# Optimization experiments

Measured on AMD Instinct MI355X. Metric: run time of the kernel, lower is better.

## Reference

```python
import jax, jax.numpy as jnp
import numpy as np

B, J, O = 32, 20, 20
D, H, F, L = 256, 8, 1024, 6
S = J * O
DH = D // H
NL = L + 1  # 6 encoder blocks + final block stacked together


def setup_inputs() -> dict:
    ks = jax.random.split(jax.random.key(0), 16)
    s = 0.02
    am = jax.random.randint(ks[4], (B, J), 0, 2) == 1
    am = am.at[:, 0].set(False)  # at least one unmasked job per row (avoid all -inf softmax)
    return {
        "operations": jax.random.normal(ks[0], (B, J, O, 2), jnp.float32),
        "job_ops_mask": jax.random.normal(ks[1], (B, J, O, O), jnp.float32),
        "ops_machines_mask": jax.random.normal(ks[2], (B, S, S), jnp.float32),
        "jobs_next_op_idx": jax.random.randint(ks[3], (B, J, 1), 0, O),
        "action_mask": am,
        "qkv_w": jax.random.normal(ks[5], (NL, 3 * D, D), jnp.float32) * s,
        "qkv_b": jnp.zeros((NL, 3 * D), jnp.float32),
        "out_w": jax.random.normal(ks[6], (NL, D, D), jnp.float32) * s,
        "out_b": jnp.zeros((NL, D), jnp.float32),
        "ln1_g": jnp.ones((NL, D), jnp.float32),
        "ln1_b": jnp.zeros((NL, D), jnp.float32),
        "ln2_g": jnp.ones((NL, D), jnp.float32),
        "ln2_b": jnp.zeros((NL, D), jnp.float32),
        "ff1_w": jax.random.normal(ks[7], (NL, F, D), jnp.float32) * s,
        "ff1_b": jnp.zeros((NL, F), jnp.float32),
        "ff2_w": jax.random.normal(ks[8], (NL, D, F), jnp.float32) * s,
        "ff2_b": jnp.zeros((NL, D), jnp.float32),
        "op_emb_w": jax.random.normal(ks[9], (D, 2), jnp.float32) * s,
        "op_emb_b": jnp.zeros((D,), jnp.float32),
        "pol_w": jax.random.normal(ks[10], (1, D), jnp.float32) * s,
        "pol_b": jnp.zeros((1,), jnp.float32),
    }


def _ln(x, g, b):
    m = x.mean(-1, keepdims=True)
    v = ((x - m) ** 2).mean(-1, keepdims=True)
    return (x - m) * jax.lax.rsqrt(v + 1e-5) * g + b


def _mha(x, mask, qw, qb, ow, ob):
    N, Sq, _ = x.shape
    qkv = x @ qw.T + qb
    q, k, v = jnp.split(qkv, 3, axis=-1)
    q = q.reshape(N, Sq, H, DH).transpose(0, 2, 1, 3)
    k = k.reshape(N, Sq, H, DH).transpose(0, 2, 1, 3)
    v = v.reshape(N, Sq, H, DH).transpose(0, 2, 1, 3)
    sc = jnp.einsum("nhqd,nhkd->nhqk", q, k) / jnp.sqrt(jnp.float32(DH))
    sc = sc + mask  # additive float attn mask, broadcast over heads where needed
    a = jax.nn.softmax(sc, axis=-1)
    o = jnp.einsum("nhqk,nhkd->nhqd", a, v).transpose(0, 2, 1, 3).reshape(N, Sq, D)
    return o @ ow.T + ob


def _forward(operations, job_ops_mask, ops_machines_mask, jobs_next_op_idx, action_mask,
             qkv_w, qkv_b, out_w, out_b, ln1_g, ln1_b, ln2_g, ln2_b,
             ff1_w, ff1_b, ff2_w, ff2_b, op_emb_w, op_emb_b, pol_w, pol_b):
    def block(x, mask, i):  # pre-norm TransformerEncoderLayer, gelu, dropout=0
        h = _ln(x, ln1_g[i], ln1_b[i])
        x = x + _mha(h, mask, qkv_w[i], qkv_b[i], out_w[i], out_b[i])
        h = _ln(x, ln2_g[i], ln2_b[i])
        ff = jax.nn.gelu(h @ ff1_w[i].T + ff1_b[i], approximate=False) @ ff2_w[i].T + ff2_b[i]
        return x + ff

    # sinusoidal positional encoding over the operation index
    pos = jnp.arange(O, dtype=jnp.float32)[:, None]
    div = jnp.exp(jnp.arange(0, D, 2, dtype=jnp.float32) * (-np.log(10000.0) / D))
    pe = jnp.stack([jnp.sin(pos * div), jnp.cos(pos * div)], axis=-1).reshape(O, D)
    x = operations @ op_emb_w.T + op_emb_b + pe[None, None]  # (B,J,O,D)

    # ALiBi slopes: 1/x^(i+1), x = 256^(1/H)
    base = (2.0 ** 8) ** (1.0 / H)
    slope = (1.0 / base ** jnp.arange(1, H + 1, dtype=jnp.float32))[None, :, None, None]
    job_mask = job_ops_mask.reshape(B * J, 1, O, O) * slope  # (B*J, H, O, O)
    mach_mask = ops_machines_mask[:, None, :, :]  # (B, 1, S, S), identical across heads

    for i in range(L):
        if i % 2 == 0:  # per-job attention over operations
            x = block(x.reshape(B * J, O, D), job_mask, i).reshape(B, J, O, D)
        else:  # per-machine attention over all operations
            x = block(x.reshape(B, S, D), mach_mask, i).reshape(B, J, O, D)

    idx = jnp.broadcast_to(jobs_next_op_idx[:, :, :, None], (B, J, 1, D))
    nxt = jnp.take_along_axis(x, idx, axis=2)[:, :, 0, :]  # (B, J, D)
    kp = jnp.where(action_mask, -jnp.inf, 0.0)[:, None, None, :]  # key padding mask
    nxt = block(nxt, kp, L)
    logits = (nxt @ pol_w.T + pol_b)[:, :, 0]
    return jnp.where(action_mask, -jnp.inf, logits)


def reference(operations, job_ops_mask, ops_machines_mask, jobs_next_op_idx, action_mask,
              qkv_w, qkv_b, out_w, out_b, ln1_g, ln1_b, ln2_g, ln2_b,
              ff1_w, ff1_b, ff2_w, ff2_b, op_emb_w, op_emb_b, pol_w, pol_b):
    return _forward(operations, job_ops_mask, ops_machines_mask, jobs_next_op_idx, action_mask,
                    qkv_w, qkv_b, out_w, out_b, ln1_g, ln1_b, ln2_g, ln2_b,
                    ff1_w, ff1_b, ff2_w, ff2_b, op_emb_w, op_emb_b, pol_w, pol_b)
```

## Files before the change

### kernel.cpp

```cpp
#include <hip/hip_runtime.h>
#include <math.h>

#define B_  32
#define J_  20
#define O_  20
#define S_  400
#define D_  256
#define H_  8
#define F_  1024
#define L_  6
#define T_  12800
#define T2_ 640

#define NEG_BIG (-1e30f)

typedef __attribute__((ext_vector_type(8))) short short8;
typedef __attribute__((ext_vector_type(4))) float f32x4;

__device__ __forceinline__ short f2b(float f) {
  union { float f; unsigned u; } c; c.f = f;
  unsigned r = (c.u + 0x7FFFu + ((c.u >> 16) & 1u)) >> 16;
  return (short)r;
}
__device__ __forceinline__ float b2f(short s) {
  union { unsigned u; float f; } c;
  c.u = ((unsigned)(unsigned short)s) << 16;
  return c.f;
}
__device__ __forceinline__ unsigned addpk(unsigned a, unsigned b) {
  union { unsigned u; float f; } x, y;
  x.u = a << 16;        y.u = b << 16;        float lo = x.f + y.f;
  x.u = a & 0xffff0000u; y.u = b & 0xffff0000u; float hi = x.f + y.f;
  return (unsigned)(unsigned short)f2b(lo) | ((unsigned)(unsigned short)f2b(hi) << 16);
}
__device__ __forceinline__ void async_copy16(const short* g, short* l) {
  __builtin_amdgcn_global_load_lds(
      (const __attribute__((address_space(1))) void*)g,
      (__attribute__((address_space(3))) void*)l, 16, 0, 0);
}

__global__ __launch_bounds__(256) void k_f2b4(
    const float* __restrict__ s0, short* __restrict__ d0,
    const float* __restrict__ s1, short* __restrict__ d1,
    const float* __restrict__ s2, short* __restrict__ d2,
    const float* __restrict__ s3, short* __restrict__ d3,
    const float* __restrict__ s4, short* __restrict__ d4)
{
  int bid = blockIdx.x;
  const float* src; short* dst; int base;
  if (bid < 672)        { src = s0; dst = d0; base = bid; }
  else if (bid < 896)   { src = s1; dst = d1; base = bid - 672; }
  else if (bid < 1792)  { src = s2; dst = d2; base = bid - 896; }
  else if (bid < 2688)  { src = s3; dst = d3; base = bid - 1792; }
  else                  { src = s4; dst = d4; base = bid - 2688; }
  int i = (base * 256 + threadIdx.x) * 8;
  float4 a = *(const float4*)(src + i);
  float4 b = *(const float4*)(src + i + 4);
  short8 o;
  o[0] = f2b(a.x); o[1] = f2b(a.y); o[2] = f2b(a.z); o[3] = f2b(a.w);
  o[4] = f2b(b.x); o[5] = f2b(b.y); o[6] = f2b(b.z); o[7] = f2b(b.w);
  *(short8*)(dst + i) = o;
}

__global__ __launch_bounds__(640) void k_maskconv(
    const void* __restrict__ am_raw, int* __restrict__ am_out)
{
  __shared__ int isInt32;
  const int tid = threadIdx.x;
  if (tid == 0) isInt32 = 1;
  __syncthreads();
  if (tid < 160) {
    int v = ((const int*)am_raw)[tid];
    if (v != 0 && v != 1) atomicAnd(&isInt32, 0);
  }
  __syncthreads();
  if (tid < 640) {
    int v;
    if (isInt32) v = ((const int*)am_raw)[tid] != 0;
    else         v = ((const unsigned char*)am_raw)[tid] != 0;
    am_out[tid] = v;
  }
}

__global__ __launch_bounds__(256) void k_embed(
    const float* __restrict__ ops, const float* __restrict__ ew,
    const float* __restrict__ eb, short* __restrict__ x)
{
  int idx = blockIdx.x * 256 + threadIdx.x;
  int d = idx & 255;
  int t = idx >> 8;
  int o = t % O_;
  float a0 = ops[(size_t)t * 2 + 0], a1 = ops[(size_t)t * 2 + 1];
  int k = d >> 1;
  float div = expf((float)(2 * k) * -0.03597789207803197f);
  float ang = (float)o * div;
  float pe = (d & 1) ? cosf(ang) : sinf(ang);
  x[idx] = f2b(a0 * ew[d * 2 + 0] + a1 * ew[d * 2 + 1] + eb[d] + pe);
}

__global__ __launch_bounds__(256) void k_ln(
    const short* __restrict__ x, const float* __restrict__ g, const float* __restrict__ b,
    short* __restrict__ out, int nTok)
{
  int gid = blockIdx.x * 256 + threadIdx.x;
  int tok = gid >> 6, lane = threadIdx.x & 63;
  if (tok >= nTok) return;
  int2 pk = ((const int2*)(x + (size_t)tok * 256))[lane];
  union { unsigned u; float f; } c;
  float vx, vy, vz, vw;
  c.u = (unsigned)pk.x << 16;        vx = c.f;
  c.u = (unsigned)pk.x & 0xffff0000u; vy = c.f;
  c.u = (unsigned)pk.y << 16;        vz = c.f;
  c.u = (unsigned)pk.y & 0xffff0000u; vw = c.f;
  float s = vx + vy + vz + vw;
  #pragma unroll
  for (int off = 32; off > 0; off >>= 1) s += __shfl_down(s, off);
  float mean = __shfl(s, 0) * (1.f / 256.f);
  float dx = vx - mean, dy = vy - mean, dz = vz - mean, dw = vw - mean;
  float q = dx * dx + dy * dy + dz * dz + dw * dw;
  #pragma unroll
  for (int off = 32; off > 0; off >>= 1) q += __shfl_down(q, off);
  float var = __shfl(q, 0) * (1.f / 256.f);
  float inv = 1.f / sqrtf(var + 1e-5f);
  float4 gv = ((const float4*)g)[lane];
  float4 bv = ((const float4*)b)[lane];
  float ox = dx * inv * gv.x + bv.x;
  float oy = dy * inv * gv.y + bv.y;
  float oz = dz * inv * gv.z + bv.z;
  float ow = dw * inv * gv.w + bv.w;
  int2 po;
  po.x = (int)(unsigned short)f2b(ox) | ((int)(unsigned short)f2b(oy) << 16);
  po.y = (int)(unsigned short)f2b(oz) | ((int)(unsigned short)f2b(ow) << 16);
  ((int2*)(out + (size_t)tok * 256))[lane] = po;
}

__global__ __launch_bounds__(256) void k_gemm_bf16(
    const short* __restrict__ A, const short* __restrict__ W,
    const float* __restrict__ bias, const short* __restrict__ R,
    short* __restrict__ C, int M, int N, int K, int act)
{
  __shared__ short LDS_[17408];
  short* Asf = LDS_;
  short* Bsf = LDS_ + 8192;
  short* Csf = LDS_;
  const int tid  = threadIdx.x;
  const int lane = tid & 63;
  const int wv   = tid >> 6;
  const int lm   = lane & 15;
  const int quad = lane >> 4;
  const int wm   = (wv >> 1) * 64;
  const int wn   = (wv & 1) * 64;
  const int n0 = blockIdx.x * 128;
  const int m0 = blockIdx.y * 128;

  f32x4 acc[4][4] = {};

  for (int k0 = 0; k0 < K; k0 += 64) {
    __syncthreads();
    #pragma unroll
    for (int i = 0; i < 4; ++i) {
      const int c    = tid + 256 * i;
      const int row  = c >> 3;
      const int kc8  = ((c & 7) ^ (row & 7)) * 8;
      async_copy16(A + (size_t)(m0 + row) * K + k0 + kc8, &Asf[c * 8]);
      async_copy16(W + (size_t)(n0 + row) * K + k0 + kc8, &Bsf[c * 8]);
    }
    __syncthreads();
    #pragma unroll
    for (int kh = 0; kh < 2; ++kh) {
      short8 af[4], bf[4];
      #pragma unroll
      for (int i = 0; i < 4; ++i) {
        const int row  = wm + i * 16 + lm;
        const int slot = (kh * 4 + quad) ^ (lm & 7);
        af[i] = *(short8*)&Asf[(row * 8 + slot) * 8];
      }
      #pragma unroll
      for (int j = 0; j < 4; ++j) {
        const int row  = wn + j * 16 + lm;
        const int slot = (kh * 4 + quad) ^ (lm & 7);
        bf[j] = *(short8*)&Bsf[(row * 8 + slot) * 8];
      }
      #pragma unroll
      for (int i = 0; i < 4; ++i)
        #pragma unroll
        for (int j = 0; j < 4; ++j)
          acc[i][j] = __builtin_amdgcn_mfma_f32_16x16x32_bf16(af[i], bf[j], acc[i][j], 0, 0, 0);
    }
  }

  __syncthreads();
  #pragma unroll
  for (int j = 0; j < 4; ++j) {
    const int ccol = wn + j * 16 + lm;
    const float bv = bias[n0 + ccol];
    #pragma unroll
    for (int i = 0; i < 4; ++i) {
      #pragma unroll
      for (int r = 0; r < 4; ++r) {
        const int row = wm + i * 16 + quad * 4 + r;
        float vvv = acc[i][j][r] + bv;
        if (act) vvv = vvv / (1.f + __expf(-1.702f * vvv));
        Csf[row * 136 + ccol] = f2b(vvv);
      }
    }
  }
  __syncthreads();
  {
    const int srow = tid >> 1, sh = (tid & 1) * 64;
    const size_t gbase = (size_t)(m0 + srow) * N + n0 + sh;
    const short* ls = &Csf[srow * 136 + sh];
    #pragma unroll
    for (int u = 0; u < 8; ++u) {
      uint4 v = *(const uint4*)(ls + u * 8);
      if (R) {
        uint4 rv = *(const uint4*)(R + gbase + u * 8);
        v.x = addpk(v.x, rv.x); v.y = addpk(v.y, rv.y);
        v.z = addpk(v.z, rv.z); v.w = addpk(v.w, rv.w);
      }
      *(uint4*)(C + gbase + u * 8) = v;
    }
  }
}

__global__ __launch_bounds__(256) void k_gemm_ln(
    const short* __restrict__ A, const short* __restrict__ W,
    const float* __restrict__ bias, const short* __restrict__ R,
    short* __restrict__ X, short* __restrict__ Hout,
    const float* __restrict__ g, const float* __restrict__ bb_,
    int M, int K)
{
  __shared__ short LDS_[4096 + 16896];
  short* Asf = LDS_;
  short* Bsf = LDS_ + 4096;
  short* Csf = LDS_ + 4096;
  const int tid  = threadIdx.x;
  const int lane = tid & 63;
  const int wv   = tid >> 6;
  const int lm   = lane & 15;
  const int quad = lane >> 4;
  const int wn   = wv * 64;
  const int m0   = blockIdx.x * 64;

  f32x4 acc[4][4] = {};

  for (int k0 = 0; k0 < K; k0 += 64) {
    __syncthreads();
    #pragma unroll
    for (int i = 0; i < 2; ++i) {
      const int c   = tid + 256 * i;
      const int row = c >> 3;
      const int kc8 = ((c & 7) ^ (row & 7)) * 8;
      async_copy16(A + (size_t)(m0 + row) * K + k0 + kc8, &Asf[c * 8]);
    }
    #pragma unroll
    for (int i = 0; i < 8; ++i) {
      const int c   = tid + 256 * i;
      const int row = c >> 3;
      const int kc8 = ((c & 7) ^ (row & 7)) * 8;
      async_copy16(W + (size_t)row * K + k0 + kc8, &Bsf[c * 8]);
    }
    __syncthreads();
    #pragma unroll
    for (int kh = 0; kh < 2; ++kh) {
      short8 af[4], bf[4];
      #pragma unroll
      for (int i = 0; i < 4; ++i) {
        const int row  = i * 16 + lm;
        const int slot = (kh * 4 + quad) ^ (lm & 7);
        af[i] = *(short8*)&Asf[(row * 8 + slot) * 8];
      }
      #pragma unroll
      for (int j = 0; j < 4; ++j) {
        const int row  = wn + j * 16 + lm;
        const int slot = (kh * 4 + quad) ^ (lm & 7);
        bf[j] = *(short8*)&Bsf[(row * 8 + slot) * 8];
      }
      #pragma unroll
      for (int i = 0; i < 4; ++i)
        #pragma unroll
        for (int j = 0; j < 4; ++j)
          acc[i][j] = __builtin_amdgcn_mfma_f32_16x16x32_bf16(af[i], bf[j], acc[i][j], 0, 0, 0);
    }
  }

  __syncthreads();
  #pragma unroll
  for (int j = 0; j < 4; ++j) {
    const int ccol = wn + j * 16 + lm;
    const float bv = bias[ccol];
    #pragma unroll
    for (int i = 0; i < 4; ++i) {
      #pragma unroll
      for (int r = 0; r < 4; ++r) {
        const int row = i * 16 + quad * 4 + r;
        Csf[row * 264 + ccol] = f2b(acc[i][j][r] + bv);
      }
    }
  }
  __syncthreads();

  {
    const int row = tid >> 2, cb = (tid & 3) * 64;
    const size_t gbase = (size_t)(m0 + row) * 256 + cb;
    const short* ls = &Csf[row * 264 + cb];
    uint4 xv[8];
    float s1 = 0.f, s2 = 0.f;
    #pragma unroll
    for (int u = 0; u < 8; ++u) {
      uint4 v = *(const uint4*)(ls + u * 8);
      uint4 rv = *(const uint4*)(R + gbase + u * 8);
      v.x = addpk(v.x, rv.x); v.y = addpk(v.y, rv.y);
      v.z = addpk(v.z, rv.z); v.w = addpk(v.w, rv.w);
      xv[u] = v;
      *(uint4*)(X + gbase + u * 8) = v;
      #pragma unroll
      for (int w2 = 0; w2 < 4; ++w2) {
        unsigned pv = (&v.x)[w2];
        union { unsigned u; float f; } c1, c2;
        c1.u = pv << 16; c2.u = pv & 0xffff0000u;
        s1 += c1.f + c2.f;
        s2 += c1.f * c1.f + c2.f * c2.f;
      }
    }
    s1 += __shfl_xor(s1, 1); s2 += __shfl_xor(s2, 1);
    s1 += __shfl_xor(s1, 2); s2 += __shfl_xor(s2, 2);
    const float mean = s1 * (1.f / 256.f);
    const float var  = s2 * (1.f / 256.f) - mean * mean;
    const float inv  = 1.f / sqrtf(var + 1e-5f);
    #pragma unroll
    for (int u = 0; u < 8; ++u) {
      float4 g0 = *(const float4*)(g + cb + u * 8);
      float4 g1 = *(const float4*)(g + cb + u * 8 + 4);
      float4 b0 = *(const float4*)(bb_ + cb + u * 8);
      float4 b1 = *(const float4*)(bb_ + cb + u * 8 + 4);
      auto lnpk = [&](unsigned pv, float ga, float gb2, float ba, float bb2) -> unsigned {
        union { unsigned u; float f; } c1, c2;
        c1.u = pv << 16; c2.u = pv & 0xffff0000u;
        float lo = (c1.f - mean) * inv * ga + ba;
        float hi = (c2.f - mean) * inv * gb2 + bb2;
        return (unsigned)(unsigned short)f2b(lo) | ((unsigned)(unsigned short)f2b(hi) << 16);
      };
      uint4 hv;
      hv.x = lnpk(xv[u].x, g0.x, g0.y, b0.x, b0.y);
      hv.y = lnpk(xv[u].y, g0.z, g0.w, b0.z, b0.w);
      hv.z = lnpk(xv[u].z, g1.x, g1.y, b1.x, b1.y);
      hv.w = lnpk(xv[u].w, g1.z, g1.w, b1.z, b1.w);
      *(uint4*)(Hout + gbase + u * 8) = hv;
    }
  }
}

#define QSTR 776
#define PSTR20 40
__global__ __launch_bounds__(512) void k_attn20_mfma(
    const short* __restrict__ qkv, short* __restrict__ att,
    const float* __restrict__ jmask, const int* __restrict__ amask, int mode)
{
  __shared__ short QK[32 * QSTR];
  __shared__ short Ps[8][32 * PSTR20];
  const int seq  = blockIdx.x;
  const int tid  = threadIdx.x;
  const int wv   = tid >> 6;
  const int lane = tid & 63;
  const int l15  = lane & 15;
  const int quad = lane >> 4;
  const float scale = 0.1767766952966369f;

  for (int e = tid; e < 3072; e += 512) {
    int row = e / 96, c8 = (e % 96) * 8;
    uint4 v = {0u, 0u, 0u, 0u};
    if (row < 20) v = *(const uint4*)(qkv + ((size_t)seq * 20 + row) * 768 + c8);
    *(uint4*)&QK[row * QSTR + c8] = v;
  }
  __syncthreads();

  const short8 aq0 = *(short8*)&QK[(0  + l15) * QSTR + wv * 32 + quad * 8];
  const short8 aq1 = *(short8*)&QK[(16 + l15) * QSTR + wv * 32 + quad * 8];
  const short8 bk0 = *(short8*)&QK[(0  + l15) * QSTR + 256 + wv * 32 + quad * 8];
  const short8 bk1 = *(short8*)&QK[(16 + l15) * QSTR + 256 + wv * 32 + quad * 8];
  f32x4 z4 = {0.f, 0.f, 0.f, 0.f};
  f32x4 s00 = __builtin_amdgcn_mfma_f32_16x16x32_bf16(aq0, bk0, z4, 0, 0, 0);
  f32x4 s01 = __builtin_amdgcn_mfma_f32_16x16x32_bf16(aq0, bk1, z4, 0, 0, 0);
  f32x4 s10 = __builtin_amdgcn_mfma_f32_16x16x32_bf16(aq1, bk0, z4, 0, 0, 0);
  f32x4 s11 = __builtin_amdgcn_mfma_f32_16x16x32_bf16(aq1, bk1, z4, 0, 0, 0);

  const float slope = exp2f(-(float)(wv + 1));
  short* psw = &Ps[wv][0];
  float l0[4] = {0.f, 0.f, 0.f, 0.f};
  float l1[4] = {0.f, 0.f, 0.f, 0.f};

  #pragma unroll
  for (int kt = 0; kt < 2; ++kt) {
    const int k  = kt * 16 + l15;
    const int kc = (k < 20) ? k : 19;
    float madd1 = 0.f;
    if (mode == 1) madd1 = amask[seq * 20 + kc] ? NEG_BIG : 0.f;
    #pragma unroll
    for (int qt = 0; qt < 2; ++qt) {
      f32x4 s = (kt == 0) ? (qt == 0 ? s00 : s10) : (qt == 0 ? s01 : s11);
      #pragma unroll
      for (int r = 0; r < 4; ++r) {
        const int q  = qt * 16 + quad * 4 + r;
        const int qc = (q < 20) ? q : 19;
        float sv = s[r] * scale;
        if (mode == 0) sv += jmask[(size_t)seq * 400 + qc * 20 + kc] * slope;
        else           sv += madd1;
        float p = (k < 20) ? __expf(fminf(sv, 40.f)) : 0.f;
        if (qt == 0) l0[r] += p; else l1[r] += p;
        psw[q * PSTR20 + k] = f2b(p);
      }
    }
  }
  #pragma unroll
  for (int r = 0; r < 4; ++r) {
    float t0 = l0[r];
    t0 += __shfl_xor(t0, 1); t0 += __shfl_xor(t0, 2);
    t0 += __shfl_xor(t0, 4); t0 += __shfl_xor(t0, 8);
    l0[r] = 1.f / t0;
    float t1 = l1[r];
    t1 += __shfl_xor(t1, 1); t1 += __shfl_xor(t1, 2);
    t1 += __shfl_xor(t1, 4); t1 += __shfl_xor(t1, 8);
    l1[r] = 1.f / t1;
  }

  const short8 pf0 = *(short8*)&psw[(0  + l15) * PSTR20 + quad * 8];
  const short8 pf1 = *(short8*)&psw[(16 + l15) * PSTR20 + quad * 8];
  #pragma unroll
  for (int dt = 0; dt < 2; ++dt) {
    const int d = wv * 32 + dt * 16 + l15;
    short8 vf;
    #pragma unroll
    for (int j = 0; j < 8; ++j)
      vf[j] = QK[(quad * 8 + j) * QSTR + 512 + d];
    f32x4 o0 = __builtin_amdgcn_mfma_f32_16x16x32_bf16(pf0, vf, z4, 0, 0, 0);
    f32x4 o1 = __builtin_amdgcn_mfma_f32_16x16x32_bf16(pf1, vf, z4, 0, 0, 0);
    #pragma unroll
    for (int r = 0; r < 4; ++r) {
      const int q = quad * 4 + r;
      att[((size_t)seq * 20 + q) * 256 + d] = f2b(o0[r] * l0[r]);
    }
    if (quad == 0) {
      #pragma unroll
      for (int r = 0; r < 4; ++r) {
        const int q = 16 + r;
        att[((size_t)seq * 20 + q) * 256 + d] = f2b(o1[r] * l1[r]);
      }
    }
  }
}

#define VTS 416
__global__ __launch_bounds__(256) void k_vtrans(
    const short* __restrict__ qkv, short* __restrict__ vt)
{
  __shared__ short T[64][73];
  const int bid = blockIdx.x;
  const int b  = bid / 28, rem = bid % 28;
  const int kt = rem / 4, dt = rem % 4;
  const int k0 = kt * 64, d0 = dt * 64;
  const int tid = threadIdx.x;
  #pragma unroll
  for (int i = 0; i < 2; ++i) {
    const int c = tid + 256 * i;
    const int row = c >> 3, cc = (c & 7) * 8;
    const int tok = k0 + row;
    uint4 v = {0u, 0u, 0u, 0u};
    if (tok < 400)
      v = *(const uint4*)(qkv + ((size_t)(b * 400 + tok)) * 768 + 512 + d0 + cc);
    *(uint4*)&T[row][cc] = v;
  }
  __syncthreads();
  #pragma unroll
  for (int i = 0; i < 2; ++i) {
    const int c = tid + 256 * i;
    const int dl = c >> 3, kk = (c & 7) * 8;
    if (k0 + kk < VTS) {
      short8 o;
      #pragma unroll
      for (int j = 0; j < 8; ++j) o[j] = T[kk + j][dl];
      *(short8*)(vt + ((size_t)(b * 256 + d0 + dl)) * VTS + k0 + kk) = o;
    }
  }
}

#define PSTRW 40
#define MSTR 424
__global__ __launch_bounds__(512) void k_attn400_mfma(
    const short* __restrict__ qkv, const short* __restrict__ vt,
    short* __restrict__ att, const short* __restrict__ mbf)
{
  __shared__ short Pl[8][16 * PSTRW];
  __shared__ short Ml[16 * MSTR];

  const int id   = blockIdx.x;
  const int b    = (id >> 3) / 25 * 8 + (id & 7);
  const int qt   = (id >> 3) % 25;
  const int tid  = threadIdx.x;
  const int wv   = tid >> 6;
  const int lane = tid & 63;
  const int l15  = lane & 15;
  const int quad = lane >> 4;
  const int q0   = qt * 16;
  const float scale = 0.1767766952966369f;

  for (int e = tid; e < 16 * 52; e += 512) {
    const int row = e / 52, cc = e % 52;
    uint4 v = {0u, 0u, 0u, 0u};
    if (cc < 50)
      v = *(const uint4*)(mbf + ((size_t)(b * 400 + q0 + row)) * 400 + cc * 8);
    *(uint4*)&Ml[row * MSTR + cc * 8] = v;
  }

  short* Pw = &Pl[wv][0];
  const short* qbase = qkv + (size_t)b * 400 * 768;
  const short* vtb   = vt + ((size_t)b * 256 + wv * 32) * VTS;

  const short8 af = *(const short8*)(qbase + (size_t)(q0 + l15) * 768 + wv * 32 + quad * 8);

  f32x4 accO[2] = {};
  float lsum = 0.f;

  short8 kf0, kf1, nvf0, nvf1;
  auto prefK = [&](int k0) {
    kf0 = *(const short8*)(qbase + (size_t)(k0 + l15) * 768 + 256 + wv * 32 + quad * 8);
    int kr = k0 + 16 + l15; if (kr > 399) kr = 399;
    kf1 = *(const short8*)(qbase + (size_t)kr * 768 + 256 + wv * 32 + quad * 8);
  };
  auto prefV = [&](int k0) {
    nvf0 = *(const short8*)(vtb + (size_t)(0  + l15) * VTS + k0 + quad * 8);
    nvf1 = *(const short8*)(vtb + (size_t)(16 + l15) * VTS + k0 + quad * 8);
  };
  prefK(0);
  prefV(0);

  __syncthreads();

  const short* mrow = &Ml[l15 * MSTR];

  for (int k0 = 0; k0 < 416; k0 += 32) {
    const short8 ck0 = kf0, ck1 = kf1;
    const short8 cv0 = nvf0, cv1 = nvf1;

    f32x4 z4 = {0.f, 0.f, 0.f, 0.f};
    f32x4 s0 = __builtin_amdgcn_mfma_f32_16x16x32_bf16(ck0, af, z4, 0, 0, 0);
    f32x4 s1 = __builtin_amdgcn_mfma_f32_16x16x32_bf16(ck1, af, z4, 0, 0, 0);

    if (k0 + 32 < 416) { prefK(k0 + 32); prefV(k0 + 32); }

    uint2 ma = *(const uint2*)(mrow + k0 + quad * 4);
    uint2 mb = *(const uint2*)(mrow + k0 + 16 + quad * 4);
    float mAv[4], mBv[4];
    {
      union { unsigned u; float f; } c;
      c.u = ma.x << 16;         mAv[0] = c.f;
      c.u = ma.x & 0xffff0000u; mAv[1] = c.f;
      c.u = ma.y << 16;         mAv[2] = c.f;
      c.u = ma.y & 0xffff0000u; mAv[3] = c.f;
      c.u = mb.x << 16;         mBv[0] = c.f;
      c.u = mb.x & 0xffff0000u; mBv[1] = c.f;
      c.u = mb.y << 16;         mBv[2] = c.f;
      c.u = mb.y & 0xffff0000u; mBv[3] = c.f;
    }

    float p0[4], p1[4];
    #pragma unroll
    for (int r = 0; r < 4; ++r) {
      const int kB = k0 + 16 + quad * 4 + r;
      float svA = s0[r] * scale + mAv[r];
      float svB = (kB < 400) ? (s1[r] * scale + mBv[r]) : NEG_BIG;
      p0[r] = __expf(fminf(svA, 40.f));
      p1[r] = __expf(fminf(svB, 40.f));
      lsum += p0[r] + p1[r];
    }

    unsigned pk00, pk01, pk10, pk11;
    asm("v_cvt_pk_bf16_f32 %0, %1, %2" : "=v"(pk00) : "v"(p0[0]), "v"(p0[1]));
    asm("v_cvt_pk_bf16_f32 %0, %1, %2" : "=v"(pk01) : "v"(p0[2]), "v"(p0[3]));
    asm("v_cvt_pk_bf16_f32 %0, %1, %2" : "=v"(pk10) : "v"(p1[0]), "v"(p1[1]));
    asm("v_cvt_pk_bf16_f32 %0, %1, %2" : "=v"(pk11) : "v"(p1[2]), "v"(p1[3]));
    uint2 w0; w0.x = pk00; w0.y = pk01;
    uint2 w1; w1.x = pk10; w1.y = pk11;
    *(uint2*)&Pw[l15 * PSTRW + quad * 4]      = w0;
    *(uint2*)&Pw[l15 * PSTRW + 16 + quad * 4] = w1;
    const short8 pf = *(short8*)&Pw[l15 * PSTRW + quad * 8];

    accO[0] = __builtin_amdgcn_mfma_f32_16x16x32_bf16(cv0, pf, accO[0], 0, 0, 0);
    accO[1] = __builtin_amdgcn_mfma_f32_16x16x32_bf16(cv1, pf, accO[1], 0, 0, 0);
  }

  lsum += __shfl_xor(lsum, 16);
  lsum += __shfl_xor(lsum, 32);
  const float inv = 1.f / lsum;

  #pragma unroll
  for (int c = 0; c < 2; ++c) {
    float a0 = accO[c][0] * inv, a1 = accO[c][1] * inv;
    float a2 = accO[c][2] * inv, a3 = accO[c][3] * inv;
    unsigned o01, o23;
    asm("v_cvt_pk_bf16_f32 %0, %1, %2" : "=v"(o01) : "v"(a0), "v"(a1));
    asm("v_cvt_pk_bf16_f32 %0, %1, %2" : "=v"(o23) : "v"(a2), "v"(a3));
    uint2 ov; ov.x = o01; ov.y = o23;
    *(uint2*)&att[((size_t)b * 400 + q0 + l15) * 256 + wv * 32 + c * 16 + quad * 4] = ov;
  }
}

__global__ __launch_bounds__(256) void k_gather2(
    const short* __restrict__ x, const short* __restrict__ h,
    const int* __restrict__ idx, short* __restrict__ x2, short* __restrict__ h2)
{
  int t = blockIdx.x * 256 + threadIdx.x;
  if (t >= 640 * 16) return;
  int bj = t >> 4, c = t & 15;
  int o = idx[bj];
  size_t src = ((size_t)bj * 20 + o) * 256;
  ((uint4*)(x2 + (size_t)bj * 256))[c] = ((const uint4*)(x + src))[c];
  ((uint4*)(h2 + (size_t)bj * 256))[c] = ((const uint4*)(h + src))[c];
}

__global__ __launch_bounds__(256) void k_logits(
    const short* __restrict__ x2, const float* __restrict__ pw, const float* __restrict__ pb,
    const int* __restrict__ am, float* __restrict__ out)
{
  int gid = blockIdx.x * 256 + threadIdx.x;
  int row = gid >> 6, lane = threadIdx.x & 63;
  int2 pk = ((const int2*)(x2 + (size_t)row * 256))[lane];
  union { unsigned u; float f; } c;
  float vx, vy, vz, vw;
  c.u = (unsigned)pk.x << 16;         vx = c.f;
  c.u = (unsigned)pk.x & 0xffff0000u; vy = c.f;
  c.u = (unsigned)pk.y << 16;         vz = c.f;
  c.u = (unsigned)pk.y & 0xffff0000u; vw = c.f;
  float4 w = ((const float4*)pw)[lane];
  float s = vx * w.x + vy * w.y + vz * w.z + vw * w.w;
  #pragma unroll
  for (int off = 32; off > 0; off >>= 1) s += __shfl_down(s, off);
  if (lane == 0) out[row] = am[row] ? NEG_BIG : (s + pb[0]);
}

extern "C" void kernel_launch(void* const* d_in, const int* in_sizes, int n_in,
                              void* d_out, int out_size, void* d_ws, size_t ws_size,
                              hipStream_t stream)
{
  (void)in_sizes; (void)n_in; (void)out_size; (void)ws_size;
  const float* operations        = (const float*)d_in[0];
  const float* job_ops_mask      = (const float*)d_in[1];
  const float* ops_machines_mask = (const float*)d_in[2];
  const int*   jobs_next_op_idx  = (const int*)d_in[3];
  const void*  action_mask_raw   = (const void*)d_in[4];
  const float* qkv_w = (const float*)d_in[5];
  const float* qkv_b = (const float*)d_in[6];
  const float* out_w = (const float*)d_in[7];
  const float* out_b = (const float*)d_in[8];
  const float* ln1_g = (const float*)d_in[9];
  const float* ln1_b = (const float*)d_in[10];
  const float* ln2_g = (const float*)d_in[11];
  const float* ln2_b = (const float*)d_in[12];
  const float* ff1_w = (const float*)d_in[13];
  const float* ff1_b = (const float*)d_in[14];
  const float* ff2_w = (const float*)d_in[15];
  const float* ff2_b = (const float*)d_in[16];
  const float* op_emb_w = (const float*)d_in[17];
  const float* op_emb_b = (const float*)d_in[18];
  const float* pol_w = (const float*)d_in[19];
  const float* pol_b = (const float*)d_in[20];
  float* out = (float*)d_out;

  short* x    = (short*)d_ws;
  short* x2   = x + (size_t)T_ * D_;
  short* h    = x2 + (size_t)T2_ * D_;
  short* big  = h + (size_t)T_ * D_;
  short* h2   = big + (size_t)T_ * F_;
  short* big2 = h2 + (size_t)T2_ * D_;
  int*   amc  = (int*)(big2 + (size_t)T2_ * F_);
  short* bwq  = (short*)(amc + 640);
  short* bwo  = bwq + (size_t)7 * 768 * 256;
  short* bwf1 = bwo + (size_t)7 * 256 * 256;
  short* bwf2 = bwf1 + (size_t)7 * 1024 * 256;
  short* mbf  = bwf2 + (size_t)7 * 256 * 1024;
  short* vt   = mbf + (size_t)B_ * 400 * 400;

  auto gemm = [&](const short* A, const short* Wb, const float* bias, const short* R,
                  short* C, int M, int N, int K, int act) {
    k_gemm_bf16<<<dim3(N / 128, M / 128), dim3(256), 0, stream>>>(
        A, Wb, bias, R, C, M, N, K, act);
  };
  auto gemm_ln = [&](const short* A, const short* Wb, const float* bias, const short* R,
                     short* X, short* Hout, const float* g, const float* b, int M, int K) {
    k_gemm_ln<<<dim3(M / 64), dim3(256), 0, stream>>>(
        A, Wb, bias, R, X, Hout, g, b, M, K);
  };

  k_f2b4<<<dim3(5188), 256, 0, stream>>>(qkv_w, bwq, out_w, bwo, ff1_w, bwf1,
                                         ff2_w, bwf2, ops_machines_mask, mbf);
  k_maskconv<<<dim3(1), dim3(640), 0, stream>>>(action_mask_raw, amc);
  k_embed<<<dim3(T_ * D_ / 256), dim3(256), 0, stream>>>(operations, op_emb_w, op_emb_b, x);
  k_ln<<<dim3(T_ / 4), 256, 0, stream>>>(x, ln1_g, ln1_b, h, T_);

  for (int i = 0; i < L_; ++i) {
    const short* qw  = bwq  + (size_t)i * 768 * 256;
    const float* qb  = qkv_b + (size_t)i * 768;
    const short* ow  = bwo  + (size_t)i * 256 * 256;
    const float* ob  = out_b + (size_t)i * 256;
    const short* f1w = bwf1 + (size_t)i * 1024 * 256;
    const float* f1b = ff1_b + (size_t)i * 1024;
    const short* f2w = bwf2 + (size_t)i * 256 * 1024;
    const float* f2b_ = ff2_b + (size_t)i * 256;
    gemm(h, qw, qb, nullptr, big, T_, 768, 256, 0);
    if ((i & 1) == 0) {
      k_attn20_mfma<<<dim3(640), 512, 0, stream>>>(big, h, job_ops_mask, nullptr, 0);
    } else {
      k_vtrans<<<dim3(896), 256, 0, stream>>>(big, vt);
      k_attn400_mfma<<<dim3(800), 512, 0, stream>>>(big, vt, h, mbf);
    }
    gemm_ln(h, ow, ob, x, x, h, ln2_g + i * D_, ln2_b + i * D_, T_, 256);
    gemm(h, f1w, f1b, nullptr, big, T_, 1024, 256, 1);
    gemm_ln(big, f2w, f2b_, x, x, h, ln1_g + (i + 1) * D_, ln1_b + (i + 1) * D_, T_, 1024);
  }

  k_gather2<<<dim3(40), 256, 0, stream>>>(x, h, jobs_next_op_idx, x2, h2);

  {
    int i = L_;
    const short* qw  = bwq  + (size_t)i * 768 * 256;
    const float* qb  = qkv_b + (size_t)i * 768;
    const short* ow  = bwo  + (size_t)i * 256 * 256;
    const float* ob  = out_b + (size_t)i * 256;
    const short* f1w = bwf1 + (size_t)i * 1024 * 256;
    const float* f1b = ff1_b + (size_t)i * 1024;
    const short* f2w = bwf2 + (size_t)i * 256 * 1024;
    const float* f2b_ = ff2_b + (size_t)i * 256;
    gemm(h2, qw, qb, nullptr, big2, T2_, 768, 256, 0);
    k_attn20_mfma<<<dim3(32), 512, 0, stream>>>(big2, h2, nullptr, amc, 1);
    gemm_ln(h2, ow, ob, x2, x2, h2, ln2_g + i * D_, ln2_b + i * D_, T2_, 256);
    gemm(h2, f1w, f1b, nullptr, big2, T2_, 1024, 256, 1);
    gemm(big2, f2w, f2b_, x2, x2, T2_, 256, 1024, 0);
  }

  k_logits<<<dim3(160), 256, 0, stream>>>(x2, pol_w, pol_b, amc, out);
}
```

Baseline: 961.0 us.

## Process 32 queries per block in 400-token attention with double-buffered K/V prefetch

The per-machine attention kernel now handles two 16-row query tiles per block. Each loaded K and V fragment is reused for two query tiles, which halves K/V global traffic per query and cuts the grid from 800 to 416 blocks. K/V prefetch becomes two-deep, alternating buffers across a manually unrolled loop. In exchange, each thread holds more registers and there are fewer blocks to fill the GPU. The last tile of 16 padded rows does redundant work, and those rows are clamped on load and masked on store.

After: 931.9 us. 3.0% less time.

```diff
diff --git a/kernel.cpp b/kernel.cpp
--- a/kernel.cpp
+++ b/kernel.cpp
@@ -490,118 +490,156 @@
     const short* __restrict__ qkv, const short* __restrict__ vt,
     short* __restrict__ att, const short* __restrict__ mbf)
 {
-  __shared__ short Pl[8][16 * PSTRW];
-  __shared__ short Ml[16 * MSTR];
+  __shared__ short Pl[8][2 * 16 * PSTRW];
+  __shared__ short Ml[32 * MSTR];
 
   const int id   = blockIdx.x;
-  const int b    = (id >> 3) / 25 * 8 + (id & 7);
-  const int qt   = (id >> 3) % 25;
+  const int b    = (id & 7) + 8 * ((id >> 3) / 13);
+  const int qt   = (id >> 3) % 13;
   const int tid  = threadIdx.x;
   const int wv   = tid >> 6;
   const int lane = tid & 63;
   const int l15  = lane & 15;
   const int quad = lane >> 4;
-  const int q0   = qt * 16;
+  const int q0   = qt * 32;
   const float scale = 0.1767766952966369f;
 
-  for (int e = tid; e < 16 * 52; e += 512) {
+  for (int e = tid; e < 32 * 52; e += 512) {
     const int row = e / 52, cc = e % 52;
+    const int srow = (q0 + row < 400) ? (q0 + row) : 399;
     uint4 v = {0u, 0u, 0u, 0u};
     if (cc < 50)
-      v = *(const uint4*)(mbf + ((size_t)(b * 400 + q0 + row)) * 400 + cc * 8);
+      v = *(const uint4*)(mbf + ((size_t)(b * 400 + srow)) * 400 + cc * 8);
     *(uint4*)&Ml[row * MSTR + cc * 8] = v;
   }
 
-  short* Pw = &Pl[wv][0];
+  short* Pw0 = &Pl[wv][0];
+  short* Pw1 = &Pl[wv][16 * PSTRW];
   const short* qbase = qkv + (size_t)b * 400 * 768;
   const short* vtb   = vt + ((size_t)b * 256 + wv * 32) * VTS;
 
-  const short8 af = *(const short8*)(qbase + (size_t)(q0 + l15) * 768 + wv * 32 + quad * 8);
-
-  f32x4 accO[2] = {};
-  float lsum = 0.f;
-
-  short8 kf0, kf1, nvf0, nvf1;
-  auto prefK = [&](int k0) {
-    kf0 = *(const short8*)(qbase + (size_t)(k0 + l15) * 768 + 256 + wv * 32 + quad * 8);
-    int kr = k0 + 16 + l15; if (kr > 399) kr = 399;
-    kf1 = *(const short8*)(qbase + (size_t)kr * 768 + 256 + wv * 32 + quad * 8);
-  };
-  auto prefV = [&](int k0) {
-    nvf0 = *(const short8*)(vtb + (size_t)(0  + l15) * VTS + k0 + quad * 8);
-    nvf1 = *(const short8*)(vtb + (size_t)(16 + l15) * VTS + k0 + quad * 8);
-  };
-  prefK(0);
-  prefV(0);
-
-  __syncthreads();
-
-  const short* mrow = &Ml[l15 * MSTR];
-
-  for (int k0 = 0; k0 < 416; k0 += 32) {
-    const short8 ck0 = kf0, ck1 = kf1;
-    const short8 cv0 = nvf0, cv1 = nvf1;
-
-    f32x4 z4 = {0.f, 0.f, 0.f, 0.f};
-    f32x4 s0 = __builtin_amdgcn_mfma_f32_16x16x32_bf16(ck0, af, z4, 0, 0, 0);
-    f32x4 s1 = __builtin_amdgcn_mfma_f32_16x16x32_bf16(ck1, af, z4, 0, 0, 0);
-
-    if (k0 + 32 < 416) { prefK(k0 + 32); prefV(k0 + 32); }
-
-    uint2 ma = *(const uint2*)(mrow + k0 + quad * 4);
-    uint2 mb = *(const uint2*)(mrow + k0 + 16 + quad * 4);
-    float mAv[4], mBv[4];
-    {
-      union { unsigned u; float f; } c;
-      c.u = ma.x << 16;         mAv[0] = c.f;
-      c.u = ma.x & 0xffff0000u; mAv[1] = c.f;
-      c.u = ma.y << 16;         mAv[2] = c.f;
-      c.u = ma.y & 0xffff0000u; mAv[3] = c.f;
-      c.u = mb.x << 16;         mBv[0] = c.f;
-      c.u = mb.x & 0xffff0000u; mBv[1] = c.f;
-      c.u = mb.y << 16;         mBv[2] = c.f;
-      c.u = mb.y & 0xffff0000u; mBv[3] = c.f;
-    }
-
-    float p0[4], p1[4];
-    #pragma unroll
-    for (int r = 0; r < 4; ++r) {
-      const int kB = k0 + 16 + quad * 4 + r;
-      float svA = s0[r] * scale + mAv[r];
-      float svB = (kB < 400) ? (s1[r] * scale + mBv[r]) : NEG_BIG;
-      p0[r] = __expf(fminf(svA, 40.f));
-      p1[r] = __expf(fminf(svB, 40.f));
-      lsum += p0[r] + p1[r];
-    }
-
-    unsigned pk00, pk01, pk10, pk11;
-    asm("v_cvt_pk_bf16_f32 %0, %1, %2" : "=v"(pk00) : "v"(p0[0]), "v"(p0[1]));
-    asm("v_cvt_pk_bf16_f32 %0, %1, %2" : "=v"(pk01) : "v"(p0[2]), "v"(p0[3]));
-    asm("v_cvt_pk_bf16_f32 %0, %1, %2" : "=v"(pk10) : "v"(p1[0]), "v"(p1[1]));
-    asm("v_cvt_pk_bf16_f32 %0, %1, %2" : "=v"(pk11) : "v"(p1[2]), "v"(p1[3]));
-    uint2 w0; w0.x = pk00; w0.y = pk01;
-    uint2 w1; w1.x = pk10; w1.y = pk11;
-    *(uint2*)&Pw[l15 * PSTRW + quad * 4]      = w0;
-    *(uint2*)&Pw[l15 * PSTRW + 16 + quad * 4] = w1;
-    const short8 pf = *(short8*)&Pw[l15 * PSTRW + quad * 8];
-
-    accO[0] = __builtin_amdgcn_mfma_f32_16x16x32_bf16(cv0, pf, accO[0], 0, 0, 0);
-    accO[1] = __builtin_amdgcn_mfma_f32_16x16x32_bf16(cv1, pf, accO[1], 0, 0, 0);
-  }
-
-  lsum += __shfl_xor(lsum, 16);
-  lsum += __shfl_xor(lsum, 32);
-  const float inv = 1.f / lsum;
-
-  #pragma unroll
-  for (int c = 0; c < 2; ++c) {
-    float a0 = accO[c][0] * inv, a1 = accO[c][1] * inv;
-    float a2 = accO[c][2] * inv, a3 = accO[c][3] * inv;
-    unsigned o01, o23;
-    asm("v_cvt_pk_bf16_f32 %0, %1, %2" : "=v"(o01) : "v"(a0), "v"(a1));
-    asm("v_cvt_pk_bf16_f32 %0, %1, %2" : "=v"(o23) : "v"(a2), "v"(a3));
-    uint2 ov; ov.x = o01; ov.y = o23;
-    *(uint2*)&att[((size_t)b * 400 + q0 + l15) * 256 + wv * 32 + c * 16 + quad * 4] = ov;
+  const short8 af0 = *(const short8*)(qbase + (size_t)(q0 + l15) * 768 + wv * 32 + quad * 8);
+  int aq1 = q0 + 16 + l15; if (aq1 > 399) aq1 = 399;
+  const short8 af1 = *(const short8*)(qbase + (size_t)aq1 * 768 + wv * 32 + quad * 8);
+
+  f32x4 accO[2][2] = {};
+  float lsum0 = 0.f, lsum1 = 0.f;
+
+  short8 kA0, kA1, vA0, vA1, kB0, kB1, vB0, vB1;
+
+#define PREFKV(K0, KF0, KF1, VF0, VF1)                                          \
+  {                                                                             \
+    KF0 = *(const short8*)(qbase + (size_t)((K0) + l15) * 768 + 256 + wv * 32 + quad * 8); \
+    int kr_ = (K0) + 16 + l15; if (kr_ > 399) kr_ = 399;                        \
+    KF1 = *(const short8*)(qbase + (size_t)kr_ * 768 + 256 + wv * 32 + quad * 8); \
+    VF0 = *(const short8*)(vtb + (size_t)(0  + l15) * VTS + (K0) + quad * 8);   \
+    VF1 = *(const short8*)(vtb + (size_t)(16 + l15) * VTS + (K0) + quad * 8);   \
+  }
+
+#define BODY(K0, KF0, KF1, VF0, VF1)                                            \
+  {                                                                             \
+    f32x4 z4 = {0.f, 0.f, 0.f, 0.f};                                            \
+    f32x4 s00 = __builtin_amdgcn_mfma_f32_16x16x32_bf16(KF0, af0, z4, 0, 0, 0); \
+    f32x4 s01 = __builtin_amdgcn_mfma_f32_16x16x32_bf16(KF1, af0, z4, 0, 0, 0); \
+    f32x4 s10 = __builtin_amdgcn_mfma_f32_16x16x32_bf16(KF0, af1, z4, 0, 0, 0); \
+    f32x4 s11 = __builtin_amdgcn_mfma_f32_16x16x32_bf16(KF1, af1, z4, 0, 0, 0); \
+    const short* mr0 = &Ml[l15 * MSTR];                                         \
+    const short* mr1 = &Ml[(16 + l15) * MSTR];                                  \
+    uint2 ma0 = *(const uint2*)(mr0 + (K0) + quad * 4);                         \
+    uint2 mb0 = *(const uint2*)(mr0 + (K0) + 16 + quad * 4);                    \
+    uint2 ma1 = *(const uint2*)(mr1 + (K0) + quad * 4);                         \
+    uint2 mb1 = *(const uint2*)(mr1 + (K0) + 16 + quad * 4);                    \
+    float p00[4], p01[4], p10[4], p11[4];                                       \
+    _Pragma("unroll")                                                           \
+    for (int r = 0; r < 4; ++r) {                                               \
+      const int kB = (K0) + 16 + quad * 4 + r;                                  \
+      union { unsigned u; float f; } cm;                                        \
+      unsigned wa0 = (r < 2) ? ma0.x : ma0.y;                                   \
+      unsigned wb0 = (r < 2) ? mb0.x : mb0.y;                                   \
+      unsigned wa1 = (r < 2) ? ma1.x : ma1.y;                                   \
+      unsigned wb1 = (r < 2) ? mb1.x : mb1.y;                                   \
+      cm.u = (r & 1) ? (wa0 & 0xffff0000u) : (wa0 << 16); float mA0 = cm.f;     \
+      cm.u = (r & 1) ? (wb0 & 0xffff0000u) : (wb0 << 16); float mB0 = cm.f;     \
+      cm.u = (r & 1) ? (wa1 & 0xffff0000u) : (wa1 << 16); float mA1 = cm.f;     \
+      cm.u = (r & 1) ? (wb1 & 0xffff0000u) : (wb1 << 16); float mB1 = cm.f;     \
+      float sA0 = s00[r] * scale + mA0;                                         \
+      float sB0 = (kB < 400) ? (s01[r] * scale + mB0) : NEG_BIG;                \
+      float sA1 = s10[r] * scale + mA1;                                         \
+      float sB1 = (kB < 400) ? (s11[r] * scale + mB1) : NEG_BIG;                \
+      p00[r] = __expf(fminf(sA0, 40.f));                                        \
+      p01[r] = __expf(fminf(sB0, 40.f));                                        \
+      p10[r] = __expf(fminf(sA1, 40.f));                                        \
+      p11[r] = __expf(fminf(sB1, 40.f));                                        \
+      lsum0 += p00[r] + p01[r];                                                 \
+      lsum1 += p10[r] + p11[r];                                                 \
+    }                                                                           \
+    unsigned q00, q01, q02, q03, q10, q11, q12, q13;                            \
+    asm("v_cvt_pk_bf16_f32 %0, %1, %2" : "=v"(q00) : "v"(p00[0]), "v"(p00[1]));  \
+    asm("v_cvt_pk_bf16_f32 %0, %1, %2" : "=v"(q01) : "v"(p00[2]), "v"(p00[3]));  \
+    asm("v_cvt_pk_bf16_f32 %0, %1, %2" : "=v"(q02) : "v"(p01[0]), "v"(p01[1]));  \
+    asm("v_cvt_pk_bf16_f32 %0, %1, %2" : "=v"(q03) : "v"(p01[2]), "v"(p01[3]));  \
+    asm("v_cvt_pk_bf16_f32 %0, %1, %2" : "=v"(q10) : "v"(p10[0]), "v"(p10[1]));  \
+    asm("v_cvt_pk_bf16_f32 %0, %1, %2" : "=v"(q11) : "v"(p10[2]), "v"(p10[3]));  \
+    asm("v_cvt_pk_bf16_f32 %0, %1, %2" : "=v"(q12) : "v"(p11[0]), "v"(p11[1]));  \
+    asm("v_cvt_pk_bf16_f32 %0, %1, %2" : "=v"(q13) : "v"(p11[2]), "v"(p11[3]));  \
+    uint2 w00; w00.x = q00; w00.y = q01;                                        \
+    uint2 w01; w01.x = q02; w01.y = q03;                                        \
+    uint2 w10; w10.x = q10; w10.y = q11;                                        \
+    uint2 w11; w11.x = q12; w11.y = q13;                                        \
+    *(uint2*)&Pw0[l15 * PSTRW + quad * 4]      = w00;                           \
+    *(uint2*)&Pw0[l15 * PSTRW + 16 + quad * 4] = w01;                           \
+    *(uint2*)&Pw1[l15 * PSTRW + quad * 4]      = w10;                           \
+    *(uint2*)&Pw1[l15 * PSTRW + 16 + quad * 4] = w11;                           \
+    const short8 pf0 = *(short8*)&Pw0[l15 * PSTRW + quad * 8];                  \
+    const short8 pf1 = *(short8*)&Pw1[l15 * PSTRW + quad * 8];                  \
+    accO[0][0] = __builtin_amdgcn_mfma_f32_16x16x32_bf16(VF0, pf0, accO[0][0], 0, 0, 0); \
+    accO[0][1] = __builtin_amdgcn_mfma_f32_16x16x32_bf16(VF1, pf0, accO[0][1], 0, 0, 0); \
+    accO[1][0] = __builtin_amdgcn_mfma_f32_16x16x32_bf16(VF0, pf1, accO[1][0], 0, 0, 0); \
+    accO[1][1] = __builtin_amdgcn_mfma_f32_16x16x32_bf16(VF1, pf1, accO[1][1], 0, 0, 0); \
+  }
+
+  PREFKV(0, kA0, kA1, vA0, vA1)
+  PREFKV(32, kB0, kB1, vB0, vB1)
+
+  __syncthreads();
+
+  int k0 = 0;
+  #pragma unroll 1
+  for (int it = 0; it < 6; ++it) {
+    BODY(k0, kA0, kA1, vA0, vA1)
+    if (k0 + 64 < 416) PREFKV(k0 + 64, kA0, kA1, vA0, vA1)
+    k0 += 32;
+    BODY(k0, kB0, kB1, vB0, vB1)
+    if (k0 + 64 < 416) PREFKV(k0 + 64, kB0, kB1, vB0, vB1)
+    k0 += 32;
+  }
+  BODY(k0, kA0, kA1, vA0, vA1)
+
+#undef PREFKV
+#undef BODY
+
+  lsum0 += __shfl_xor(lsum0, 16);
+  lsum0 += __shfl_xor(lsum0, 32);
+  lsum1 += __shfl_xor(lsum1, 16);
+  lsum1 += __shfl_xor(lsum1, 32);
+  const float inv0 = 1.f / lsum0;
+  const float inv1 = 1.f / lsum1;
+
+  #pragma unroll
+  for (int qh = 0; qh < 2; ++qh) {
+    const int q = q0 + qh * 16 + l15;
+    if (q >= 400) continue;
+    const float inv = qh ? inv1 : inv0;
+    #pragma unroll
+    for (int c = 0; c < 2; ++c) {
+      float a0 = accO[qh][c][0] * inv, a1 = accO[qh][c][1] * inv;
+      float a2 = accO[qh][c][2] * inv, a3 = accO[qh][c][3] * inv;
+      unsigned o01, o23;
+      asm("v_cvt_pk_bf16_f32 %0, %1, %2" : "=v"(o01) : "v"(a0), "v"(a1));
+      asm("v_cvt_pk_bf16_f32 %0, %1, %2" : "=v"(o23) : "v"(a2), "v"(a3));
+      uint2 ov; ov.x = o01; ov.y = o23;
+      *(uint2*)&att[((size_t)b * 400 + q) * 256 + wv * 32 + c * 16 + quad * 4] = ov;
+    }
   }
 }
 
@@ -711,7 +749,7 @@
       k_attn20_mfma<<<dim3(640), 512, 0, stream>>>(big, h, job_ops_mask, nullptr, 0);
     } else {
       k_vtrans<<<dim3(896), 256, 0, stream>>>(big, vt);
-      k_attn400_mfma<<<dim3(800), 512, 0, stream>>>(big, vt, h, mbf);
+      k_attn400_mfma<<<dim3(416), 512, 0, stream>>>(big, vt, h, mbf);
     }
     gemm_ln(h, ow, ob, x, x, h, ln2_g + i * D_, ln2_b + i * D_, T_, 256);
     gemm(h, f1w, f1b, nullptr, big, T_, 1024, 256, 1);
```
